# Optimization experiments

Measured on AMD Instinct MI355X. Metric: run time of the kernel, lower is better.

Reference implementation:

```python
import jax, jax.numpy as jnp
import numpy as np

N = 100000
E = 1600000
IN_DIM = 256
OUT_DIM = 128
LEAKY_SLOPE = 0.01  # torch nn.LeakyReLU default


def setup_inputs() -> dict:
    key = jax.random.key(0)
    k1, k2, k3, k4, k5 = jax.random.split(key, 5)
    features = jax.random.normal(k1, (N, IN_DIM), dtype=jnp.float32)
    # xavier_uniform for weight [out, in]
    limit = float(np.sqrt(6.0 / (IN_DIM + OUT_DIM)))
    weight = jax.random.uniform(k2, (OUT_DIM, IN_DIM), dtype=jnp.float32,
                                minval=-limit, maxval=limit)
    edge_rows = jnp.sort(jax.random.randint(k3, (E,), 0, N, dtype=jnp.int32))
    edge_cols = jax.random.randint(k4, (E,), 0, N, dtype=jnp.int32)
    edge_vals = jax.random.uniform(k5, (E,), dtype=jnp.float32)
    return {"features": features, "weight": weight,
            "edge_rows": edge_rows, "edge_cols": edge_cols,
            "edge_vals": edge_vals}


def reference(features, weight, edge_rows, edge_cols, edge_vals):
    # support = LeakyReLU(features @ W^T)   [N, OUT_DIM]
    support = jax.nn.leaky_relu(jnp.einsum('ni,oi->no', features, weight),
                                negative_slope=LEAKY_SLOPE)
    # SpMM: out[r] = sum over edges (r, c, v) of v * support[c]
    msgs = support[edge_cols] * edge_vals[:, None]  # [E, OUT_DIM]
    out = jax.ops.segment_sum(msgs, edge_rows, num_segments=N)
    return out
```

## Files before the change

### kernel.cpp

```cpp
#include <hip/hip_runtime.h>

#define IN_DIM 256
#define OUT_DIM 128
#define LEAKY 0.01f

typedef __attribute__((ext_vector_type(8))) short bf16x8;
typedef __attribute__((ext_vector_type(4))) float f32x4;

__device__ inline unsigned cvtpk_bf16(float lo, float hi) {
  unsigned r;
  asm volatile("v_cvt_pk_bf16_f32 %0, %1, %2" : "=v"(r) : "v"(lo), "v"(hi));
  return r;
}

__device__ inline float b2f(unsigned short u) {
  union { unsigned u; float f; } c;
  c.u = ((unsigned)u) << 16;
  return c.f;
}

__device__ inline int swz_byte(int r, int u) {
  return r * 512 + ((u & 16) << 4) + (((u & 15) ^ (r & 15)) << 4);
}

__global__ __launch_bounds__(256) void wcvt(const float* __restrict__ w,
                                            unsigned* __restrict__ wbf) {
  int i = blockIdx.x * 256 + threadIdx.x;
  float2 v = reinterpret_cast<const float2*>(w)[i];
  wbf[i] = cvtpk_bf16(v.x, v.y);
}

__global__ __launch_bounds__(256) void scan_bounds(const int* __restrict__ erows,
                                                   int* __restrict__ rs,
                                                   int nrows, int nedges) {
  int i = blockIdx.x * 256 + threadIdx.x;
  if (i >= nedges) return;
  const int cur  = erows[i];
  const int prev = (i == 0) ? -1 : erows[i - 1];
  for (int r = prev + 1; r <= cur; ++r) rs[r] = i;
  if (i == nedges - 1)
    for (int r = cur + 1; r <= nrows; ++r) rs[r] = nedges;
}

__global__ __launch_bounds__(512, 4) void gemm_mfma(
    const float* __restrict__ feat, const unsigned short* __restrict__ wbf,
    unsigned short* __restrict__ support, int nrows, int ntiles) {
  __shared__ alignas(16) unsigned short wlds[128 * 256];
  char* wb = reinterpret_cast<char*>(wlds);

  const int t = threadIdx.x;
#pragma unroll
  for (int it = 0; it < 8; ++it) {
    const int g = it * 512 + t;
    const int r = g >> 5;
    const int u = g & 31;
    const uint4 v = reinterpret_cast<const uint4*>(wbf)[g];
    *reinterpret_cast<uint4*>(wb + swz_byte(r, u)) = v;
  }
  __syncthreads();

  const int wid  = t >> 6;
  const int lane = t & 63;
  const int lrow = lane & 15;
  const int hi   = lane >> 4;

  for (int tile = blockIdx.x; tile < ntiles; tile += gridDim.x) {
    const int mrow = tile * 128 + wid * 16 + lrow;
    const int mr   = mrow < nrows ? mrow : nrows - 1;
    const float* fp = feat + mr * IN_DIM + hi * 8;

    f32x4 acc[8];
#pragma unroll
    for (int nt = 0; nt < 8; ++nt) acc[nt] = (f32x4){0.f, 0.f, 0.f, 0.f};

#pragma unroll
    for (int ks = 0; ks < 8; ++ks) {
      const float4 a = *reinterpret_cast<const float4*>(fp + ks * 32);
      const float4 b = *reinterpret_cast<const float4*>(fp + ks * 32 + 4);
      union { bf16x8 v; unsigned u[4]; } bf;
      bf.u[0] = cvtpk_bf16(a.x, a.y);
      bf.u[1] = cvtpk_bf16(a.z, a.w);
      bf.u[2] = cvtpk_bf16(b.x, b.y);
      bf.u[3] = cvtpk_bf16(b.z, b.w);
      const int u = ks * 4 + hi;
#pragma unroll
      for (int nt = 0; nt < 8; ++nt) {
        const bf16x8 af = *reinterpret_cast<const bf16x8*>(
            wb + swz_byte(nt * 16 + lrow, u));
        acc[nt] = __builtin_amdgcn_mfma_f32_16x16x32_bf16(af, bf.v, acc[nt],
                                                          0, 0, 0);
      }
    }

    if (mrow < nrows) {
      unsigned short* orow = support + mrow * OUT_DIM + hi * 4;
#pragma unroll
      for (int nt = 0; nt < 8; ++nt) {
        f32x4 v = acc[nt];
        float a0 = v[0] > 0.f ? v[0] : LEAKY * v[0];
        float a1 = v[1] > 0.f ? v[1] : LEAKY * v[1];
        float a2 = v[2] > 0.f ? v[2] : LEAKY * v[2];
        float a3 = v[3] > 0.f ? v[3] : LEAKY * v[3];
        uint2 st;
        st.x = cvtpk_bf16(a0, a1);
        st.y = cvtpk_bf16(a2, a3);
        *reinterpret_cast<uint2*>(orow + nt * 16) = st;
      }
    }
  }
}

__global__ __launch_bounds__(256) void spmm_bf16(
    const int* __restrict__ rs, const int* __restrict__ ecols,
    const float* __restrict__ evals, const unsigned short* __restrict__ support,
    float* __restrict__ out, int nrows) {
  const int t    = threadIdx.x;
  const int lane = t & 31;
  const int row  = blockIdx.x * 8 + (t >> 5);
  if (row >= nrows) return;

  const int s = rs[row];
  const int e = rs[row + 1];

  f32x4 acc[8];
#pragma unroll
  for (int j = 0; j < 8; ++j) acc[j] = (f32x4){0.f, 0.f, 0.f, 0.f};

  for (int i = s; i < e; i += 8) {
    int   ii[8];
    float vv[8];
#pragma unroll
    for (int j = 0; j < 8; ++j) {
      const int  idx = i + j;
      const bool ok  = idx < e;
      ii[j] = ok ? idx : e - 1;
      vv[j] = ok ? evals[ii[j]] : 0.f;
    }
#pragma unroll
    for (int j = 0; j < 8; ++j) {
      const int c = ecols[ii[j]];
      const ushort4 u =
          *reinterpret_cast<const ushort4*>(&support[c * OUT_DIM + lane * 4]);
      acc[j].x += vv[j] * b2f(u.x);
      acc[j].y += vv[j] * b2f(u.y);
      acc[j].z += vv[j] * b2f(u.z);
      acc[j].w += vv[j] * b2f(u.w);
    }
  }

#pragma unroll
  for (int j = 1; j < 8; ++j) acc[0] += acc[j];
  __builtin_nontemporal_store(
      acc[0], reinterpret_cast<f32x4*>(&out[row * OUT_DIM + lane * 4]));
}

extern "C" void kernel_launch(void* const* d_in, const int* in_sizes, int n_in,
                              void* d_out, int out_size, void* d_ws,
                              size_t ws_size, hipStream_t stream) {
  const float* features = (const float*)d_in[0];
  const float* weight   = (const float*)d_in[1];
  const int*   erows    = (const int*)d_in[2];
  const int*   ecols    = (const int*)d_in[3];
  const float* evals    = (const float*)d_in[4];
  float*       out      = (float*)d_out;

  const int nrows  = in_sizes[0] / IN_DIM;
  const int nedges = in_sizes[2];

  unsigned short* support = (unsigned short*)d_ws;
  unsigned short* wbf =
      (unsigned short*)((char*)d_ws + (size_t)nrows * OUT_DIM * 2);
  int* rs = (int*)((char*)wbf + (size_t)OUT_DIM * IN_DIM * 2);

  const int ntiles = (nrows + 127) / 128;

  wcvt<<<64, 256, 0, stream>>>(weight, (unsigned*)wbf);
  scan_bounds<<<(nedges + 255) / 256, 256, 0, stream>>>(erows, rs, nrows,
                                                        nedges);
  gemm_mfma<<<512, 512, 0, stream>>>(features, wbf, support, nrows, ntiles);
  spmm_bf16<<<(nrows + 7) / 8, 256, 0, stream>>>(rs, ecols, evals, support,
                                                 out, nrows);
}
```

Baseline: 102.1 us.

## Fuse weight conversion and row scan into GEMM launch; widen SpMM lane loads

The separate weight-to-bf16 kernel is removed: each GEMM block now converts the fp32 weight directly while filling LDS. The row-boundary scan runs as extra blocks of the same launch as the GEMM, cutting the launch count from four to two. The SpMM gives each row 16 lanes that each load 8 bf16 values with a 16-byte load, instead of 32 lanes loading 8 bytes, to get fewer, wider gather transactions. In exchange, every GEMM block repeats the weight conversion, and the SpMM exposes less parallelism per row.

Measured after the change: 94.46 us. -7.5%, faster.

```diff
diff --git a/kernel.cpp b/kernel.cpp
--- a/kernel.cpp
+++ b/kernel.cpp
@@ -3,9 +3,11 @@
 #define IN_DIM 256
 #define OUT_DIM 128
 #define LEAKY 0.01f
+#define GEMM_BLOCKS 512
 
 typedef __attribute__((ext_vector_type(8))) short bf16x8;
 typedef __attribute__((ext_vector_type(4))) float f32x4;
+typedef __attribute__((ext_vector_type(4))) unsigned u32x4;
 
 __device__ inline unsigned cvtpk_bf16(float lo, float hi) {
   unsigned r;
@@ -13,38 +15,32 @@
   return r;
 }
 
-__device__ inline float b2f(unsigned short u) {
-  union { unsigned u; float f; } c;
-  c.u = ((unsigned)u) << 16;
-  return c.f;
+__device__ inline float blo(unsigned u) {
+  union { unsigned x; float f; } c; c.x = u << 16; return c.f;
+}
+__device__ inline float bhi(unsigned u) {
+  union { unsigned x; float f; } c; c.x = u & 0xFFFF0000u; return c.f;
 }
 
 __device__ inline int swz_byte(int r, int u) {
   return r * 512 + ((u & 16) << 4) + (((u & 15) ^ (r & 15)) << 4);
 }
 
-__global__ __launch_bounds__(256) void wcvt(const float* __restrict__ w,
-                                            unsigned* __restrict__ wbf) {
-  int i = blockIdx.x * 256 + threadIdx.x;
-  float2 v = reinterpret_cast<const float2*>(w)[i];
-  wbf[i] = cvtpk_bf16(v.x, v.y);
-}
+__global__ __launch_bounds__(512, 4) void gemm_scan(
+    const float* __restrict__ feat, const float* __restrict__ w,
+    const int* __restrict__ erows, unsigned short* __restrict__ support,
+    int* __restrict__ rs, int nrows, int nedges, int ntiles) {
+  if (blockIdx.x >= GEMM_BLOCKS) {
+    const int i = (blockIdx.x - GEMM_BLOCKS) * 512 + threadIdx.x;
+    if (i >= nedges) return;
+    const int cur  = erows[i];
+    const int prev = (i == 0) ? -1 : erows[i - 1];
+    for (int r = prev + 1; r <= cur; ++r) rs[r] = i;
+    if (i == nedges - 1)
+      for (int r = cur + 1; r <= nrows; ++r) rs[r] = nedges;
+    return;
+  }
 
-__global__ __launch_bounds__(256) void scan_bounds(const int* __restrict__ erows,
-                                                   int* __restrict__ rs,
-                                                   int nrows, int nedges) {
-  int i = blockIdx.x * 256 + threadIdx.x;
-  if (i >= nedges) return;
-  const int cur  = erows[i];
-  const int prev = (i == 0) ? -1 : erows[i - 1];
-  for (int r = prev + 1; r <= cur; ++r) rs[r] = i;
-  if (i == nedges - 1)
-    for (int r = cur + 1; r <= nrows; ++r) rs[r] = nedges;
-}
-
-__global__ __launch_bounds__(512, 4) void gemm_mfma(
-    const float* __restrict__ feat, const unsigned short* __restrict__ wbf,
-    unsigned short* __restrict__ support, int nrows, int ntiles) {
   __shared__ alignas(16) unsigned short wlds[128 * 256];
   char* wb = reinterpret_cast<char*>(wlds);
 
@@ -54,8 +50,15 @@
     const int g = it * 512 + t;
     const int r = g >> 5;
     const int u = g & 31;
-    const uint4 v = reinterpret_cast<const uint4*>(wbf)[g];
-    *reinterpret_cast<uint4*>(wb + swz_byte(r, u)) = v;
+    const float* src = w + r * IN_DIM + u * 8;
+    const float4 a = *reinterpret_cast<const float4*>(src);
+    const float4 b = *reinterpret_cast<const float4*>(src + 4);
+    uint4 pk;
+    pk.x = cvtpk_bf16(a.x, a.y);
+    pk.y = cvtpk_bf16(a.z, a.w);
+    pk.z = cvtpk_bf16(b.x, b.y);
+    pk.w = cvtpk_bf16(b.z, b.w);
+    *reinterpret_cast<uint4*>(wb + swz_byte(r, u)) = pk;
   }
   __syncthreads();
 
@@ -64,7 +67,7 @@
   const int lrow = lane & 15;
   const int hi   = lane >> 4;
 
-  for (int tile = blockIdx.x; tile < ntiles; tile += gridDim.x) {
+  for (int tile = blockIdx.x; tile < ntiles; tile += GEMM_BLOCKS) {
     const int mrow = tile * 128 + wid * 16 + lrow;
     const int mr   = mrow < nrows ? mrow : nrows - 1;
     const float* fp = feat + mr * IN_DIM + hi * 8;
@@ -115,16 +118,21 @@
     const float* __restrict__ evals, const unsigned short* __restrict__ support,
     float* __restrict__ out, int nrows) {
   const int t    = threadIdx.x;
-  const int lane = t & 31;
-  const int row  = blockIdx.x * 8 + (t >> 5);
+  const int lane = t & 15;
+  const int row  = blockIdx.x * 16 + (t >> 4);
   if (row >= nrows) return;
 
   const int s = rs[row];
   const int e = rs[row + 1];
 
-  f32x4 acc[8];
+  f32x4 accA[4], accB[4];
 #pragma unroll
-  for (int j = 0; j < 8; ++j) acc[j] = (f32x4){0.f, 0.f, 0.f, 0.f};
+  for (int j = 0; j < 4; ++j) {
+    accA[j] = (f32x4){0.f, 0.f, 0.f, 0.f};
+    accB[j] = (f32x4){0.f, 0.f, 0.f, 0.f};
+  }
+
+  const unsigned short* srow = support + lane * 8;
 
   for (int i = s; i < e; i += 8) {
     int   ii[8];
@@ -139,19 +147,29 @@
 #pragma unroll
     for (int j = 0; j < 8; ++j) {
       const int c = ecols[ii[j]];
-      const ushort4 u =
-          *reinterpret_cast<const ushort4*>(&support[c * OUT_DIM + lane * 4]);
-      acc[j].x += vv[j] * b2f(u.x);
-      acc[j].y += vv[j] * b2f(u.y);
-      acc[j].z += vv[j] * b2f(u.z);
-      acc[j].w += vv[j] * b2f(u.w);
+      const u32x4 u =
+          *reinterpret_cast<const u32x4*>(srow + (size_t)c * OUT_DIM);
+      const int   k = j & 3;
+      const float v = vv[j];
+      accA[k][0] += v * blo(u[0]);
+      accA[k][1] += v * bhi(u[0]);
+      accA[k][2] += v * blo(u[1]);
+      accA[k][3] += v * bhi(u[1]);
+      accB[k][0] += v * blo(u[2]);
+      accB[k][1] += v * bhi(u[2]);
+      accB[k][2] += v * blo(u[3]);
+      accB[k][3] += v * bhi(u[3]);
     }
   }
 
 #pragma unroll
-  for (int j = 1; j < 8; ++j) acc[0] += acc[j];
-  __builtin_nontemporal_store(
-      acc[0], reinterpret_cast<f32x4*>(&out[row * OUT_DIM + lane * 4]));
+  for (int j = 1; j < 4; ++j) {
+    accA[0] += accA[j];
+    accB[0] += accB[j];
+  }
+  float* orow = out + (size_t)row * OUT_DIM + lane * 8;
+  __builtin_nontemporal_store(accA[0], reinterpret_cast<f32x4*>(orow));
+  __builtin_nontemporal_store(accB[0], reinterpret_cast<f32x4*>(orow + 4));
 }
 
 extern "C" void kernel_launch(void* const* d_in, const int* in_sizes, int n_in,
@@ -168,16 +186,13 @@
   const int nedges = in_sizes[2];
 
   unsigned short* support = (unsigned short*)d_ws;
-  unsigned short* wbf =
-      (unsigned short*)((char*)d_ws + (size_t)nrows * OUT_DIM * 2);
-  int* rs = (int*)((char*)wbf + (size_t)OUT_DIM * IN_DIM * 2);
+  int* rs = (int*)((char*)d_ws + (size_t)nrows * OUT_DIM * 2);
 
-  const int ntiles = (nrows + 127) / 128;
+  const int ntiles      = (nrows + 127) / 128;
+  const int scan_blocks = (nedges + 511) / 512;
 
-  wcvt<<<64, 256, 0, stream>>>(weight, (unsigned*)wbf);
-  scan_bounds<<<(nedges + 255) / 256, 256, 0, stream>>>(erows, rs, nrows,
-                                                        nedges);
-  gemm_mfma<<<512, 512, 0, stream>>>(features, wbf, support, nrows, ntiles);
-  spmm_bf16<<<(nrows + 7) / 8, 256, 0, stream>>>(rs, ecols, evals, support,
-                                                 out, nrows);
+  gemm_scan<<<GEMM_BLOCKS + scan_blocks, 512, 0, stream>>>(
+      features, weight, erows, support, rs, nrows, nedges, ntiles);
+  spmm_bf16<<<(nrows + 15) / 16, 256, 0, stream>>>(rs, ecols, evals, support,
+                                                   out, nrows);
 }
```
